# Kernel tuning notes

Hardware: AMD Instinct MI355X
Metric: run time of the kernel (lower is better)

The kernel has to match this reference:

```python
import jax, jax.numpy as jnp
import numpy as np

MODES = (16, 16)

def setup_inputs() -> dict:
    key = jax.random.key(0)
    ks = jax.random.split(key, 8)
    B, Cin, Cout, H, W = 16, 64, 64, 128, 128
    scale = 1.0 / (Cin * Cout)
    return {
        "x": jax.random.normal(ks[0], (B, Cin, H, W), jnp.float32),
        "t_emb": jax.random.normal(ks[1], (B, 512), jnp.float32),
        "weight_real": jax.random.normal(ks[2], (Cin, Cout, *MODES), jnp.float32) * 2 * scale - scale,
        "weight_imag": jax.random.normal(ks[3], (Cin, Cout, *MODES), jnp.float32) * 2 * scale - scale,
        "bypass_w": jax.random.normal(ks[4], (Cout, Cin), jnp.float32) * 0.05,
        "bypass_b": jax.random.normal(ks[5], (Cout,), jnp.float32) * 0.05,
        "temb_w": jax.random.normal(ks[6], (Cin, 512), jnp.float32) * 0.02,
        "temb_b": jax.random.normal(ks[7], (Cin,), jnp.float32) * 0.02,
    }

def reference(x, t_emb, weight_real, weight_imag, bypass_w, bypass_b, temb_w, temb_b):
    mk, ml = MODES
    H, W = x.shape[-2:]
    xf = x.astype(jnp.float32)
    # truncated spectral conv: rfft2 (ortho), keep low-mode corner only
    x_fft = jnp.fft.rfftn(xf, axes=(-2, -1), norm="ortho")[:, :, :mk, :ml]
    weight = weight_real + 1j * weight_imag  # [i, o, k, l]
    out_fft = jnp.einsum("bikl,iokl->bokl", x_fft, weight)
    x_spec = jnp.fft.irfftn(out_fft, s=(H, W), axes=(-2, -1), norm="ortho")
    # 1x1 conv bypass
    byp = jnp.einsum("bihw,oi->bohw", xf, bypass_w) + bypass_b[None, :, None, None]
    out = jax.nn.gelu(x_spec + byp, approximate=False)
    # temb fusion: x + Linear(silu(temb))[:, :, None, None]
    silu_t = t_emb * jax.nn.sigmoid(t_emb)
    proj = silu_t @ temb_w.T + temb_b  # [B, C]
    out = out + proj[:, :, None, None]
    return out
```

## Files before the change

kernel.cpp:

```cpp
#include <hip/hip_runtime.h>
#include <cmath>

#define TWO_PI_128 0.04908738521234052f

typedef __attribute__((ext_vector_type(8))) short bf16x8;
typedef __attribute__((ext_vector_type(4))) float f32x4;

__device__ inline unsigned short f2bf(float v) {
  unsigned u = __float_as_uint(v);
  unsigned r = (u + 0x7FFFu + ((u >> 16) & 1u)) >> 16;
  return (unsigned short)r;
}

__global__ __launch_bounds__(256) void proj_kernel(
    const float* __restrict__ t_emb, const float* __restrict__ temb_w,
    const float* __restrict__ temb_b, float* __restrict__ proj) {
  __shared__ float s_silu[512];
  __shared__ float s_part[64][4];
  const int b = blockIdx.x;
  const int t = threadIdx.x;
  for (int j = t; j < 512; j += 256) {
    float v = t_emb[b * 512 + j];
    s_silu[j] = v / (1.f + __expf(-v));
  }
  __syncthreads();
  const int o = t >> 2, part = t & 3;
  const float* wrow = temb_w + o * 512 + part * 128;
  const float* srow = s_silu + part * 128;
  float acc = 0.f;
#pragma unroll 8
  for (int j = 0; j < 128; ++j) acc = fmaf(srow[j], wrow[j], acc);
  s_part[o][part] = acc;
  __syncthreads();
  if (part == 0) {
    proj[b * 64 + o] =
        s_part[o][0] + s_part[o][1] + s_part[o][2] + s_part[o][3] + temb_b[o];
  }
}

__global__ __launch_bounds__(256) void wtrans_kernel(
    const float* __restrict__ wr, const float* __restrict__ wi,
    float* __restrict__ wt_r, float* __restrict__ wt_i) {
  __shared__ float tile[32][33];
  const float* src = blockIdx.z ? wi : wr;
  float* dst = blockIdx.z ? wt_i : wt_r;
  const int kl0 = blockIdx.x * 32, io0 = blockIdx.y * 32;
  const int ty = threadIdx.x >> 3, tx = threadIdx.x & 7;
  float4 v = *(const float4*)(src + (size_t)(io0 + ty) * 256 + kl0 + 4 * tx);
  tile[ty][4 * tx + 0] = v.x;
  tile[ty][4 * tx + 1] = v.y;
  tile[ty][4 * tx + 2] = v.z;
  tile[ty][4 * tx + 3] = v.w;
  __syncthreads();
  float4 o;
  o.x = tile[4 * tx + 0][ty];
  o.y = tile[4 * tx + 1][ty];
  o.z = tile[4 * tx + 2][ty];
  o.w = tile[4 * tx + 3][ty];
  *(float4*)(dst + (size_t)(kl0 + ty) * 4096 + io0 + 4 * tx) = o;
}

__global__ __launch_bounds__(256) void fwd_dft_kernel(
    const float* __restrict__ x, float* __restrict__ xfr_t,
    float* __restrict__ xfi_t) {
  __shared__ float s_r[16 * 132];
  __shared__ float s_i[16 * 132];
  const int t = threadIdx.x;
  const float4* xp = (const float4*)(x + (size_t)blockIdx.x * 16384);
  const int hl = t >> 3, lp = t & 7;
  const int lb = lp + 8;
  float C0, S0, C1, S1;
  sincosf(TWO_PI_128 * (float)lp, &S0, &C0);
  sincosf(TWO_PI_128 * (float)lb, &S1, &C1);
  const float p0 = (lp & 1) ? -1.f : 1.f;

#pragma unroll
  for (int c = 0; c < 4; ++c) {
    const int row = c * 32 + hl;
    const float4* rp = xp + row * 32;
    float r0 = 0.f, i0 = 0.f, r1 = 0.f, i1 = 0.f;
    float c0 = 1.f, s0 = 0.f, c1 = 1.f, s1 = 0.f;
#pragma unroll 4
    for (int wq = 0; wq < 16; ++wq) {
      float4 xa = rp[wq], xb = rp[wq + 16];
      float xs[4] = {fmaf(p0, xb.x, xa.x), fmaf(p0, xb.y, xa.y),
                     fmaf(p0, xb.z, xa.z), fmaf(p0, xb.w, xa.w)};
#pragma unroll
      for (int m = 0; m < 4; ++m) {
        float xv = xs[m];
        r0 = fmaf(xv, c0, r0);
        i0 = fmaf(xv, -s0, i0);
        r1 = fmaf(xv, c1, r1);
        i1 = fmaf(xv, -s1, i1);
        float t0 = s0 * S0, u0 = c0 * S0;
        c0 = fmaf(c0, C0, -t0);
        s0 = fmaf(s0, C0, u0);
        float t1 = s1 * S1, u1 = c1 * S1;
        c1 = fmaf(c1, C1, -t1);
        s1 = fmaf(s1, C1, u1);
      }
    }
    s_r[lp * 132 + row] = r0;
    s_i[lp * 132 + row] = i0;
    s_r[lb * 132 + row] = r1;
    s_i[lb * 132 + row] = i1;
  }
  __syncthreads();
  const int k = t >> 4, l = t & 15;
  const float pk = (k & 1) ? -1.f : 1.f;
  float Ck, Sk;
  sincosf(TWO_PI_128 * (float)k, &Sk, &Ck);
  const float* R = s_r + l * 132;
  const float* I = s_i + l * 132;
  float Xr = 0.f, Xi = 0.f, ch = 1.f, sh = 0.f;
#pragma unroll 4
  for (int h4 = 0; h4 < 16; ++h4) {
    float4 Ra = *(const float4*)(R + 4 * h4);
    float4 Rb = *(const float4*)(R + 64 + 4 * h4);
    float4 Ia = *(const float4*)(I + 4 * h4);
    float4 Ib = *(const float4*)(I + 64 + 4 * h4);
    float ar[4] = {fmaf(pk, Rb.x, Ra.x), fmaf(pk, Rb.y, Ra.y),
                   fmaf(pk, Rb.z, Ra.z), fmaf(pk, Rb.w, Ra.w)};
    float ai[4] = {fmaf(pk, Ib.x, Ia.x), fmaf(pk, Ib.y, Ia.y),
                   fmaf(pk, Ib.z, Ia.z), fmaf(pk, Ib.w, Ia.w)};
#pragma unroll
    for (int m = 0; m < 4; ++m) {
      Xr = fmaf(ar[m], ch, Xr);
      Xr = fmaf(ai[m], sh, Xr);
      Xi = fmaf(ai[m], ch, Xi);
      Xi = fmaf(-ar[m], sh, Xi);
      float tt = sh * Sk, uu = ch * Sk;
      ch = fmaf(ch, Ck, -tt);
      sh = fmaf(sh, Ck, uu);
    }
  }
  xfr_t[(size_t)t * 1024 + blockIdx.x] = Xr * 0.0078125f;
  xfi_t[(size_t)t * 1024 + blockIdx.x] = Xi * 0.0078125f;
}

__global__ __launch_bounds__(256) void modemix_kernel(
    const float* __restrict__ xfr_t, const float* __restrict__ xfi_t,
    const float* __restrict__ wt_r, const float* __restrict__ wt_i,
    float* __restrict__ ofr, float* __restrict__ ofi) {
  __shared__ float s_xr[1024], s_xi[1024];
  __shared__ float s_wr[4096], s_wi[4096];
  const int kl = blockIdx.x;
  const int t = threadIdx.x;
  ((float4*)s_xr)[t] = ((const float4*)(xfr_t + (size_t)kl * 1024))[t];
  ((float4*)s_xi)[t] = ((const float4*)(xfi_t + (size_t)kl * 1024))[t];
  const float4* wrp = (const float4*)(wt_r + (size_t)kl * 4096);
  const float4* wip = (const float4*)(wt_i + (size_t)kl * 4096);
#pragma unroll
  for (int j = 0; j < 4; ++j) {
    ((float4*)s_wr)[t + 256 * j] = wrp[t + 256 * j];
    ((float4*)s_wi)[t + 256 * j] = wip[t + 256 * j];
  }
  __syncthreads();
  const int b0 = t >> 6;
  const int o = t & 63;
  float accr[4] = {0.f, 0.f, 0.f, 0.f};
  float acci[4] = {0.f, 0.f, 0.f, 0.f};
  for (int i = 0; i < 64; ++i) {
    float wrv = s_wr[i * 64 + o], wiv = s_wi[i * 64 + o];
#pragma unroll
    for (int j = 0; j < 4; ++j) {
      int b = b0 + 4 * j;
      float xr = s_xr[b * 64 + i], xi = s_xi[b * 64 + i];
      accr[j] = fmaf(xr, wrv, accr[j]);
      accr[j] = fmaf(-xi, wiv, accr[j]);
      acci[j] = fmaf(xr, wiv, acci[j]);
      acci[j] = fmaf(xi, wrv, acci[j]);
    }
  }
#pragma unroll
  for (int j = 0; j < 4; ++j) {
    int b = b0 + 4 * j;
    ofr[(size_t)(b * 64 + o) * 256 + kl] = accr[j];
    ofi[(size_t)(b * 64 + o) * 256 + kl] = acci[j];
  }
}

__global__ __launch_bounds__(256) void invh_kernel(
    const float* __restrict__ ofr, const float* __restrict__ ofi,
    uint4* __restrict__ Ybf) {
  __shared__ float s_fr[16 * 260], s_fi[16 * 260];
  __shared__ float2 s_tw[128];
  const int t = threadIdx.x;
  const int bid = blockIdx.x;
  const int b = bid >> 5, og = (bid >> 3) & 3, hg = bid & 7;
  if (t < 128) {
    float sv, cv;
    sincosf(TWO_PI_128 * (float)t, &sv, &cv);
    s_tw[t] = make_float2(cv, sv);
  }
#pragma unroll 4
  for (int pp = 0; pp < 16; ++pp) {
    s_fr[pp * 260 + t] = ofr[(size_t)(b * 64 + og * 16 + pp) * 256 + t];
    s_fi[pp * 260 + t] = ofi[(size_t)(b * 64 + og * 16 + pp) * 256 + t];
  }
  __syncthreads();
  const int ol = t & 15, hl = t >> 4;
  const int h = hg * 16 + hl;
  float yr[16], yi[16];
#pragma unroll
  for (int l = 0; l < 16; ++l) {
    yr[l] = 0.f;
    yi[l] = 0.f;
  }
  const float* FR = s_fr + ol * 260;
  const float* FI = s_fi + ol * 260;
  const float2 tw = s_tw[h];
  float ck = 1.f, sk = 0.f;
#pragma unroll 4
  for (int k = 0; k < 16; ++k) {
#pragma unroll
    for (int q = 0; q < 4; ++q) {
      float4 fr = *(const float4*)(FR + k * 16 + 4 * q);
      float4 fi = *(const float4*)(FI + k * 16 + 4 * q);
      int l = 4 * q;
      yr[l + 0] = fmaf(fr.x, ck, yr[l + 0]);
      yr[l + 0] = fmaf(-fi.x, sk, yr[l + 0]);
      yi[l + 0] = fmaf(fi.x, ck, yi[l + 0]);
      yi[l + 0] = fmaf(fr.x, sk, yi[l + 0]);
      yr[l + 1] = fmaf(fr.y, ck, yr[l + 1]);
      yr[l + 1] = fmaf(-fi.y, sk, yr[l + 1]);
      yi[l + 1] = fmaf(fi.y, ck, yi[l + 1]);
      yi[l + 1] = fmaf(fr.y, sk, yi[l + 1]);
      yr[l + 2] = fmaf(fr.z, ck, yr[l + 2]);
      yr[l + 2] = fmaf(-fi.z, sk, yr[l + 2]);
      yi[l + 2] = fmaf(fi.z, ck, yi[l + 2]);
      yi[l + 2] = fmaf(fr.z, sk, yi[l + 2]);
      yr[l + 3] = fmaf(fr.w, ck, yr[l + 3]);
      yr[l + 3] = fmaf(-fi.w, sk, yr[l + 3]);
      yi[l + 3] = fmaf(fi.w, ck, yi[l + 3]);
      yi[l + 3] = fmaf(fr.w, sk, yi[l + 3]);
    }
    float tt = sk * tw.y, uu = ck * tw.y;
    ck = fmaf(ck, tw.x, -tt);
    sk = fmaf(sk, tw.x, uu);
  }
  unsigned int u[16];
  {
    float sc[16];
    sc[0] = 0.0078125f;
#pragma unroll
    for (int l = 1; l < 16; ++l) sc[l] = 0.015625f;
#pragma unroll
    for (int j = 0; j < 8; ++j) {
      u[j] = (unsigned)f2bf(yr[2 * j] * sc[2 * j]) |
             ((unsigned)f2bf(yr[2 * j + 1] * sc[2 * j + 1]) << 16);
      u[8 + j] = (unsigned)f2bf(yi[2 * j] * sc[2 * j]) |
                 ((unsigned)f2bf(yi[2 * j + 1] * sc[2 * j + 1]) << 16);
    }
  }
  uint4* dst = Ybf + ((size_t)(b * 128 + h) * 64 + og * 16 + ol) * 4;
  dst[0] = make_uint4(u[0], u[1], u[2], u[3]);
  dst[1] = make_uint4(u[4], u[5], u[6], u[7]);
  dst[2] = make_uint4(u[8], u[9], u[10], u[11]);
  dst[3] = make_uint4(u[12], u[13], u[14], u[15]);
}

__global__ __launch_bounds__(256) void final_kernel(
    const float* __restrict__ x, const float* __restrict__ bw,
    const float* __restrict__ bb, const float* __restrict__ proj,
    const uint4* __restrict__ Ybf, float* __restrict__ out) {
#define AR 104
  __shared__ unsigned short s_A[64 * AR];
  __shared__ float s_bb[64];
  __shared__ float s_pb[64];
  const int h = blockIdx.x, b = blockIdx.y, t = threadIdx.x;

  if (t < 64)
    s_bb[t] = bb[t];
  else if (t < 128)
    s_pb[t - 64] = proj[b * 64 + (t - 64)];

  {
    const int o = t >> 2, q = t & 3;
    const float4* src = (const float4*)(bw + o * 64 + q * 16);
    unsigned int u[8];
#pragma unroll
    for (int m = 0; m < 4; ++m) {
      float4 v = src[m];
      u[2 * m] = (unsigned)f2bf(v.x) | ((unsigned)f2bf(v.y) << 16);
      u[2 * m + 1] = (unsigned)f2bf(v.z) | ((unsigned)f2bf(v.w) << 16);
    }
    uint4* dst = (uint4*)(s_A + o * AR + q * 16);
    dst[0] = make_uint4(u[0], u[1], u[2], u[3]);
    dst[1] = make_uint4(u[4], u[5], u[6], u[7]);
  }
  {
    const int o = t >> 2, q = t & 3;
    uint4 v = Ybf[((size_t)(b * 128 + h) * 64 + o) * 4 + q];
    *(uint4*)(s_A + o * AR + 64 + q * 8) = v;
  }
  __syncthreads();

  const int wv = t >> 6, lane = t & 63;
  const int l15 = lane & 15, quad = lane >> 4;
  const int n0w = wv * 32;

  f32x4 acc[4][2];
#pragma unroll
  for (int mt = 0; mt < 4; ++mt) {
    f32x4 bv = *(const f32x4*)(s_bb + mt * 16 + quad * 4);
    acc[mt][0] = bv;
    acc[mt][1] = bv;
  }

  const float* xrow = x + (size_t)b * 1048576 + (size_t)h * 128 + n0w + l15;
#pragma unroll
  for (int ks = 0; ks < 64; ks += 32) {
    union {
      bf16x8 v;
      unsigned short u[8];
    } bx[2];
#pragma unroll
    for (int nt = 0; nt < 2; ++nt) {
      float xv[8];
#pragma unroll
      for (int j = 0; j < 8; ++j)
        xv[j] = xrow[(size_t)(ks + quad * 8 + j) * 16384 + nt * 16];
#pragma unroll
      for (int j = 0; j < 8; ++j) bx[nt].u[j] = f2bf(xv[j]);
    }
#pragma unroll
    for (int mt = 0; mt < 4; ++mt) {
      bf16x8 a =
          *(const bf16x8*)(s_A + (mt * 16 + l15) * AR + ks + quad * 8);
      acc[mt][0] = __builtin_amdgcn_mfma_f32_16x16x32_bf16(a, bx[0].v,
                                                           acc[mt][0], 0, 0, 0);
      acc[mt][1] = __builtin_amdgcn_mfma_f32_16x16x32_bf16(a, bx[1].v,
                                                           acc[mt][1], 0, 0, 0);
    }
  }

  {
    const int lbase = (quad & 1) * 8;
    const bool iscos = (quad < 2);
    union {
      bf16x8 v;
      unsigned short u[8];
    } bs[2];
#pragma unroll
    for (int nt = 0; nt < 2; ++nt) {
      const int wn = n0w + nt * 16 + l15;
      float st, ct, ss, cc;
      sincosf(TWO_PI_128 * (float)wn, &st, &ct);
      sincosf(TWO_PI_128 * (float)(wn * lbase), &ss, &cc);
#pragma unroll
      for (int j = 0; j < 8; ++j) {
        bs[nt].u[j] = f2bf(iscos ? cc : -ss);
        float nc = cc * ct - ss * st;
        ss = ss * ct + cc * st;
        cc = nc;
      }
    }
#pragma unroll
    for (int mt = 0; mt < 4; ++mt) {
      bf16x8 a = *(const bf16x8*)(s_A + (mt * 16 + l15) * AR + 64 + quad * 8);
      acc[mt][0] = __builtin_amdgcn_mfma_f32_16x16x32_bf16(a, bs[0].v,
                                                           acc[mt][0], 0, 0, 0);
      acc[mt][1] = __builtin_amdgcn_mfma_f32_16x16x32_bf16(a, bs[1].v,
                                                           acc[mt][1], 0, 0, 0);
    }
  }

#pragma unroll
  for (int mt = 0; mt < 4; ++mt) {
    f32x4 pv = *(const f32x4*)(s_pb + mt * 16 + quad * 4);
#pragma unroll
    for (int nt = 0; nt < 2; ++nt) {
      const int wcol = n0w + nt * 16 + l15;
#pragma unroll
      for (int r = 0; r < 4; ++r) {
        const int o = mt * 16 + quad * 4 + r;
        float v = acc[mt][nt][r];
        float g = fmaf(0.5f * v, 1.f + erff(v * 0.70710678f), pv[r]);
        out[((size_t)(b * 64 + o) * 128 + h) * 128 + wcol] = g;
      }
    }
  }
#undef AR
}

extern "C" void kernel_launch(void* const* d_in, const int* in_sizes, int n_in,
                              void* d_out, int out_size, void* d_ws,
                              size_t ws_size, hipStream_t stream) {
  (void)in_sizes;
  (void)n_in;
  (void)out_size;
  (void)ws_size;
  const float* x = (const float*)d_in[0];
  const float* t_emb = (const float*)d_in[1];
  const float* wr = (const float*)d_in[2];
  const float* wi = (const float*)d_in[3];
  const float* bw = (const float*)d_in[4];
  const float* bb = (const float*)d_in[5];
  const float* tw = (const float*)d_in[6];
  const float* tb = (const float*)d_in[7];
  float* out = (float*)d_out;

  char* ws = (char*)d_ws;
  float* proj = (float*)(ws);
  float* ofr = (float*)(ws + ((size_t)1 << 20));
  float* ofi = (float*)(ws + ((size_t)2 << 20));
  float* xfr_t = (float*)(ws + ((size_t)3 << 20));
  float* xfi_t = (float*)(ws + ((size_t)4 << 20));
  float* wt_r = (float*)(ws + ((size_t)5 << 20));
  float* wt_i = (float*)(ws + ((size_t)9 << 20));
  uint4* Ybf = (uint4*)(ws + ((size_t)3 << 20));

  proj_kernel<<<16, 256, 0, stream>>>(t_emb, tw, tb, proj);
  wtrans_kernel<<<dim3(8, 128, 2), 256, 0, stream>>>(wr, wi, wt_r, wt_i);
  fwd_dft_kernel<<<1024, 256, 0, stream>>>(x, xfr_t, xfi_t);
  modemix_kernel<<<256, 256, 0, stream>>>(xfr_t, xfi_t, wt_r, wt_i, ofr, ofi);
  invh_kernel<<<512, 256, 0, stream>>>(ofr, ofi, Ybf);
  final_kernel<<<dim3(128, 16), 256, 0, stream>>>(x, bw, bb, proj, Ybf, out);
}
```

Baseline: 201.4 us.

## Compute truncated forward DFT with bf16 MFMA instead of scalar FMA recurrences

The forward truncated 2D DFT kernel is rewritten to run both passes, along W and then along H, as bf16 MFMA matrix products. Twiddle fragments are generated in registers, the intermediate goes through LDS as bf16, and partial sums from each wave are reduced in shared memory. This replaces the per-thread scalar FMA and rotation loops with matrix-core work. It lowers precision of the inputs and of the intermediate spectrum to bf16, which costs accuracy.

Result: faster. 184.6 us (-8.3%).

```diff
diff --git a/kernel.cpp b/kernel.cpp
--- a/kernel.cpp
+++ b/kernel.cpp
@@ -63,79 +63,116 @@
 __global__ __launch_bounds__(256) void fwd_dft_kernel(
     const float* __restrict__ x, float* __restrict__ xfr_t,
     float* __restrict__ xfi_t) {
-  __shared__ float s_r[16 * 132];
-  __shared__ float s_i[16 * 132];
+  __shared__ unsigned short s_x1[32 * 136];
+  __shared__ float s_red[8 * 256];
   const int t = threadIdx.x;
-  const float4* xp = (const float4*)(x + (size_t)blockIdx.x * 16384);
-  const int hl = t >> 3, lp = t & 7;
-  const int lb = lp + 8;
-  float C0, S0, C1, S1;
-  sincosf(TWO_PI_128 * (float)lp, &S0, &C0);
-  sincosf(TWO_PI_128 * (float)lb, &S1, &C1);
-  const float p0 = (lp & 1) ? -1.f : 1.f;
-
-#pragma unroll
-  for (int c = 0; c < 4; ++c) {
-    const int row = c * 32 + hl;
-    const float4* rp = xp + row * 32;
-    float r0 = 0.f, i0 = 0.f, r1 = 0.f, i1 = 0.f;
-    float c0 = 1.f, s0 = 0.f, c1 = 1.f, s1 = 0.f;
-#pragma unroll 4
-    for (int wq = 0; wq < 16; ++wq) {
-      float4 xa = rp[wq], xb = rp[wq + 16];
-      float xs[4] = {fmaf(p0, xb.x, xa.x), fmaf(p0, xb.y, xa.y),
-                     fmaf(p0, xb.z, xa.z), fmaf(p0, xb.w, xa.w)};
-#pragma unroll
-      for (int m = 0; m < 4; ++m) {
-        float xv = xs[m];
-        r0 = fmaf(xv, c0, r0);
-        i0 = fmaf(xv, -s0, i0);
-        r1 = fmaf(xv, c1, r1);
-        i1 = fmaf(xv, -s1, i1);
-        float t0 = s0 * S0, u0 = c0 * S0;
-        c0 = fmaf(c0, C0, -t0);
-        s0 = fmaf(s0, C0, u0);
-        float t1 = s1 * S1, u1 = c1 * S1;
-        c1 = fmaf(c1, C1, -t1);
-        s1 = fmaf(s1, C1, u1);
+  const int plane = blockIdx.x;
+  const int wv = t >> 6, lane = t & 63, l15 = lane & 15, quad = lane >> 4;
+
+  union U8 {
+    bf16x8 v;
+    unsigned short u[8];
+  };
+
+  float dC, dS;
+  sincosf(TWO_PI_128 * (float)l15, &dS, &dC);
+
+  U8 a_re[4], a_im[4];
+#pragma unroll
+  for (int ks = 0; ks < 4; ++ks) {
+    const int w0 = ks * 32 + quad * 8;
+    float c, s;
+    sincosf(TWO_PI_128 * (float)((l15 * w0) & 127), &s, &c);
+#pragma unroll
+    for (int j = 0; j < 8; ++j) {
+      a_re[ks].u[j] = f2bf(c);
+      a_im[ks].u[j] = f2bf(-s);
+      float nc = c * dC - s * dS;
+      s = s * dC + c * dS;
+      c = nc;
+    }
+  }
+
+  const float* xp = x + (size_t)plane * 16384;
+  f32x4 acc[2][2];
+#pragma unroll
+  for (int mt = 0; mt < 2; ++mt)
+#pragma unroll
+    for (int nt = 0; nt < 2; ++nt) acc[mt][nt] = (f32x4){0.f, 0.f, 0.f, 0.f};
+
+#pragma unroll
+  for (int ks = 0; ks < 4; ++ks) {
+#pragma unroll
+    for (int nt = 0; nt < 2; ++nt) {
+      const float* src =
+          xp + (size_t)((wv * 2 + nt) * 16 + l15) * 128 + ks * 32 + quad * 8;
+      float4 v0 = *(const float4*)src;
+      float4 v1 = *(const float4*)(src + 4);
+      U8 bx;
+      bx.u[0] = f2bf(v0.x);
+      bx.u[1] = f2bf(v0.y);
+      bx.u[2] = f2bf(v0.z);
+      bx.u[3] = f2bf(v0.w);
+      bx.u[4] = f2bf(v1.x);
+      bx.u[5] = f2bf(v1.y);
+      bx.u[6] = f2bf(v1.z);
+      bx.u[7] = f2bf(v1.w);
+      acc[0][nt] = __builtin_amdgcn_mfma_f32_16x16x32_bf16(a_re[ks].v, bx.v,
+                                                           acc[0][nt], 0, 0, 0);
+      acc[1][nt] = __builtin_amdgcn_mfma_f32_16x16x32_bf16(a_im[ks].v, bx.v,
+                                                           acc[1][nt], 0, 0, 0);
+    }
+  }
+
+#pragma unroll
+  for (int mt = 0; mt < 2; ++mt)
+#pragma unroll
+    for (int nt = 0; nt < 2; ++nt)
+#pragma unroll
+      for (int r = 0; r < 4; ++r)
+        s_x1[(mt * 16 + quad * 4 + r) * 136 + (wv * 2 + nt) * 16 + l15] =
+            f2bf(acc[mt][nt][r]);
+  __syncthreads();
+
+  f32x4 accre = (f32x4){0.f, 0.f, 0.f, 0.f};
+  f32x4 accim = (f32x4){0.f, 0.f, 0.f, 0.f};
+#pragma unroll
+  for (int kl2 = 0; kl2 < 2; ++kl2) {
+    const int ks2 = wv * 2 + kl2;
+    const int hb = (ks2 & 3) * 32 + quad * 8;
+    const int imh = ks2 >> 2;
+    float c, s;
+    sincosf(TWO_PI_128 * (float)((l15 * hb) & 127), &s, &c);
+    U8 ar, ai;
+#pragma unroll
+    for (int j = 0; j < 8; ++j) {
+      if (!imh) {
+        ar.u[j] = f2bf(c);
+        ai.u[j] = f2bf(-s);
+      } else {
+        ar.u[j] = f2bf(s);
+        ai.u[j] = f2bf(c);
       }
-    }
-    s_r[lp * 132 + row] = r0;
-    s_i[lp * 132 + row] = i0;
-    s_r[lb * 132 + row] = r1;
-    s_i[lb * 132 + row] = i1;
-  }
-  __syncthreads();
-  const int k = t >> 4, l = t & 15;
-  const float pk = (k & 1) ? -1.f : 1.f;
-  float Ck, Sk;
-  sincosf(TWO_PI_128 * (float)k, &Sk, &Ck);
-  const float* R = s_r + l * 132;
-  const float* I = s_i + l * 132;
-  float Xr = 0.f, Xi = 0.f, ch = 1.f, sh = 0.f;
-#pragma unroll 4
-  for (int h4 = 0; h4 < 16; ++h4) {
-    float4 Ra = *(const float4*)(R + 4 * h4);
-    float4 Rb = *(const float4*)(R + 64 + 4 * h4);
-    float4 Ia = *(const float4*)(I + 4 * h4);
-    float4 Ib = *(const float4*)(I + 64 + 4 * h4);
-    float ar[4] = {fmaf(pk, Rb.x, Ra.x), fmaf(pk, Rb.y, Ra.y),
-                   fmaf(pk, Rb.z, Ra.z), fmaf(pk, Rb.w, Ra.w)};
-    float ai[4] = {fmaf(pk, Ib.x, Ia.x), fmaf(pk, Ib.y, Ia.y),
-                   fmaf(pk, Ib.z, Ia.z), fmaf(pk, Ib.w, Ia.w)};
-#pragma unroll
-    for (int m = 0; m < 4; ++m) {
-      Xr = fmaf(ar[m], ch, Xr);
-      Xr = fmaf(ai[m], sh, Xr);
-      Xi = fmaf(ai[m], ch, Xi);
-      Xi = fmaf(-ar[m], sh, Xi);
-      float tt = sh * Sk, uu = ch * Sk;
-      ch = fmaf(ch, Ck, -tt);
-      sh = fmaf(sh, Ck, uu);
-    }
-  }
-  xfr_t[(size_t)t * 1024 + blockIdx.x] = Xr * 0.0078125f;
-  xfi_t[(size_t)t * 1024 + blockIdx.x] = Xi * 0.0078125f;
+      float nc = c * dC - s * dS;
+      s = s * dC + c * dS;
+      c = nc;
+    }
+    bf16x8 bfrag = *(const bf16x8*)(s_x1 + (imh * 16 + l15) * 136 + hb);
+    accre =
+        __builtin_amdgcn_mfma_f32_16x16x32_bf16(ar.v, bfrag, accre, 0, 0, 0);
+    accim =
+        __builtin_amdgcn_mfma_f32_16x16x32_bf16(ai.v, bfrag, accim, 0, 0, 0);
+  }
+  *(f32x4*)(s_red + (wv * 2) * 256 + lane * 4) = accre;
+  *(f32x4*)(s_red + (wv * 2 + 1) * 256 + lane * 4) = accim;
+  __syncthreads();
+
+  const float re = s_red[t] + s_red[512 + t] + s_red[1024 + t] + s_red[1536 + t];
+  const float im =
+      s_red[256 + t] + s_red[768 + t] + s_red[1280 + t] + s_red[1792 + t];
+  const int k = (t >> 6) * 4 + (t & 3), l = (t >> 2) & 15;
+  xfr_t[(size_t)(k * 16 + l) * 1024 + plane] = re * 0.0078125f;
+  xfi_t[(size_t)(k * 16 + l) * 1024 + plane] = im * 0.0078125f;
 }
 
 __global__ __launch_bounds__(256) void modemix_kernel(
@@ -326,8 +363,7 @@
     }
 #pragma unroll
     for (int mt = 0; mt < 4; ++mt) {
-      bf16x8 a =
-          *(const bf16x8*)(s_A + (mt * 16 + l15) * AR + ks + quad * 8);
+      bf16x8 a = *(const bf16x8*)(s_A + (mt * 16 + l15) * AR + ks + quad * 8);
       acc[mt][0] = __builtin_amdgcn_mfma_f32_16x16x32_bf16(a, bx[0].v,
                                                            acc[mt][0], 0, 0, 0);
       acc[mt][1] = __builtin_amdgcn_mfma_f32_16x16x32_bf16(a, bx[1].v,
```
